# Performance work log

Hardware: AMD Instinct MI355X
Metric: run time of the kernel (lower is better)

## Reference

```python
import jax, jax.numpy as jnp
import numpy as np

B, N, M, C = 256, 2048, 64, 512
OUT = 3 * M + 6  # fc_write output: [M,1,1,3,1,M,M]


def setup_inputs() -> dict:
    key = jax.random.key(0)
    k0, k1, k2, k3, k4 = jax.random.split(key, 5)
    xavier = 1.4 * np.sqrt(6.0 / (C + OUT))  # xavier_uniform gain=1.4 scale
    return {
        "h": jax.random.normal(k0, (B, C), jnp.float32),
        "w_prev": jax.nn.softmax(jax.random.normal(k1, (B, N), jnp.float32), axis=1),
        "memory": jax.random.normal(k2, (B, N, M), jnp.float32),
        "W": jax.random.uniform(k3, (OUT, C), jnp.float32, -xavier, xavier),
        "b": 0.01 * jax.random.normal(k4, (OUT,), jnp.float32),
    }


def reference(h, w_prev, memory, W, b):
    # controller projection + split
    o = h @ W.T + b  # [B, 3M+6]
    bounds = np.cumsum([M, 1, 1, 3, 1, M])
    k, beta, g, s, gamma, e, a = jnp.split(o, bounds, axis=1)
    beta = jax.nn.softplus(beta)            # [B,1]
    g = jax.nn.sigmoid(g)                   # [B,1]
    s = jax.nn.softmax(s, axis=1)           # [B,3] shift weights {-1,0,+1}
    gamma = 1.0 + jax.nn.softplus(gamma)    # [B,1]
    e = jax.nn.sigmoid(e)                   # [B,M]

    # content addressing: cosine similarity + softmax
    mem_e = memory + 1e-16
    k_e = k + 1e-16
    sim = jnp.einsum('bnm,bm->bn', mem_e, k_e)
    denom = jnp.maximum(
        jnp.linalg.norm(mem_e, axis=-1) * jnp.linalg.norm(k_e, axis=-1, keepdims=True),
        1e-8,
    )
    w_c = jax.nn.softmax(beta * sim / denom, axis=1)  # [B,N]

    # interpolation gate
    w_g = g * w_c + (1.0 - g) * w_prev

    # circular shift convolution (3 taps)
    w_t = (jnp.roll(w_g, 1, axis=1) * s[:, 0:1]
           + w_g * s[:, 1:2]
           + jnp.roll(w_g, -1, axis=1) * s[:, 2:3])

    # sharpening
    w_s = w_t ** gamma
    w = w_s / (jnp.sum(w_s, axis=1, keepdims=True) + 1e-16)  # [B,N]

    # erase/add memory write
    erase = jnp.einsum('bn,bm->bnm', w, e)
    add = jnp.einsum('bn,bm->bnm', w, a)
    mem_new = memory * (1.0 - erase) + add
    return w, mem_new
```

## Files before the change

kernel.cpp:

```cpp
#include <hip/hip_runtime.h>
#include <stdint.h>

#define BB   256
#define NN   2048
#define MM   64
#define CC   512
#define OUTD 198

#define CHUNK_F 4096
#define NCH     32

typedef float vf4 __attribute__((ext_vector_type(4)));

__device__ __forceinline__ float softplusf(float x) {
    return x > 20.f ? x : log1pf(expf(x));
}
__device__ __forceinline__ float sigmoidf(float x) {
    return 1.f / (1.f + expf(-x));
}

__device__ __forceinline__ void dma16(const float* g, float* l) {
    __builtin_amdgcn_global_load_lds(
        (const __attribute__((address_space(1))) uint32_t*)g,
        (__attribute__((address_space(3))) uint32_t*)l, 16, 0, 0);
}

__device__ __forceinline__ void bar_lds() {
    asm volatile("s_waitcnt lgkmcnt(0)" ::: "memory");
    __builtin_amdgcn_sched_barrier(0);
    __builtin_amdgcn_s_barrier();
    __builtin_amdgcn_sched_barrier(0);
}

__global__ __launch_bounds__(1024, 4) void k_fused(
        const float* __restrict__ h, const float* __restrict__ Wm,
        const float* __restrict__ bias, const float* __restrict__ w_prev,
        const float* __restrict__ mem, float* __restrict__ w_out,
        float* __restrict__ mem_out) {
    __shared__ __align__(16) float stage[2][CHUNK_F];
    __shared__ float hs[CC];
    __shared__ float os[OUTD];
    __shared__ __align__(16) float kk[MM];
    __shared__ __align__(16) float ee[MM];
    __shared__ __align__(16) float aa[MM];
    __shared__ float sc[8];
    __shared__ float lgs[NN];
    __shared__ float wg[NN];
    __shared__ float wprev_s[NN];
    __shared__ float red[16];

    const int b  = blockIdx.x;
    const int t  = threadIdx.x;
    const int ln = t & 63;
    const int wv = t >> 6;
    const int seg  = ln & 15;
    const int rsub = ln >> 4;

    const float* mb = mem + (size_t)b * (NN * MM);

    float hv = 0.f;
    if (t < CC) hv = h[(size_t)b * CC + t];
    const float wp0 = w_prev[(size_t)b * NN + t];
    const float wp1 = w_prev[(size_t)b * NN + t + 1024];
    dma16(mb + 0 * CHUNK_F + wv * 256 + ln * 4, &stage[0][wv * 256]);
    dma16(mb + 1 * CHUNK_F + wv * 256 + ln * 4, &stage[1][wv * 256]);
    if (t < CC) hs[t] = hv;
    wprev_s[t] = wp0;
    wprev_s[t + 1024] = wp1;
    bar_lds();

    if (t < 4 * OUTD) {
        const int row = t >> 2, l4 = t & 3;
        const float* wr = Wm + (size_t)row * CC + 4 * l4;
        float acc = 0.f;
        #pragma unroll
        for (int c = 0; c < CC; c += 16) {
            const float4 p = *(const float4*)(wr + c);
            const int hb = c + 4 * l4;
            acc += p.x * hs[hb] + p.y * hs[hb + 1] + p.z * hs[hb + 2] + p.w * hs[hb + 3];
        }
        acc += __shfl_xor(acc, 1, 64);
        acc += __shfl_xor(acc, 2, 64);
        if (l4 == 0) os[row] = acc + bias[row];
    }
    bar_lds();

    if (t < 64) {
        const float kv = os[t] + 1e-16f;
        kk[t] = kv;
        float ss = kv * kv;
        #pragma unroll
        for (int off = 32; off; off >>= 1) ss += __shfl_xor(ss, off, 64);
        if (t == 0) sc[3] = sqrtf(ss);
    } else if (t < 128) {
        const int m = t - 64;
        ee[m] = sigmoidf(os[70 + m]);
        aa[m] = os[134 + m];
    } else if (t == 128) {
        sc[0] = softplusf(os[64]);
    } else if (t == 129) {
        sc[1] = sigmoidf(os[65]);
    } else if (t == 130) {
        sc[2] = 1.f + softplusf(os[69]);
    } else if (t == 131) {
        const float x0 = os[66], x1 = os[67], x2 = os[68];
        const float mx = fmaxf(x0, fmaxf(x1, x2));
        const float e0 = expf(x0 - mx), e1 = expf(x1 - mx), e2 = expf(x2 - mx);
        const float inv = 1.f / (e0 + e1 + e2);
        sc[4] = e0 * inv; sc[5] = e1 * inv; sc[6] = e2 * inv;
    }
    bar_lds();

    {
        const float kv0 = kk[4 * seg + 0], kv1 = kk[4 * seg + 1];
        const float kv2 = kk[4 * seg + 2], kv3 = kk[4 * seg + 3];
        const float beta = sc[0], knorm = sc[3];
        for (int c = 0; c < NCH; ++c) {
            if (c < NCH - 1) { asm volatile("s_waitcnt vmcnt(1)" ::: "memory"); }
            else             { asm volatile("s_waitcnt vmcnt(0)" ::: "memory"); }
            __builtin_amdgcn_sched_barrier(0);
            const float4 p = *(const float4*)&stage[c & 1][wv * 256 + ln * 4];
            const float m0 = p.x + 1e-16f, m1 = p.y + 1e-16f;
            const float m2 = p.z + 1e-16f, m3 = p.w + 1e-16f;
            float dot = m0 * kv0 + m1 * kv1 + m2 * kv2 + m3 * kv3;
            float ss  = m0 * m0 + m1 * m1 + m2 * m2 + m3 * m3;
            #pragma unroll
            for (int off = 1; off < 16; off <<= 1) {
                dot += __shfl_xor(dot, off, 64);
                ss  += __shfl_xor(ss,  off, 64);
            }
            if (seg == 0)
                lgs[c * 64 + wv * 4 + rsub] =
                    beta * dot / fmaxf(sqrtf(ss) * knorm, 1e-8f);
            if (c + 2 < NCH)
                dma16(mb + (size_t)(c + 2) * CHUNK_F + wv * 256 + ln * 4,
                      &stage[c & 1][wv * 256]);
        }
    }
    dma16(mb + 0 * CHUNK_F + wv * 256 + ln * 4, &stage[0][wv * 256]);
    dma16(mb + 1 * CHUNK_F + wv * 256 + ln * 4, &stage[1][wv * 256]);
    bar_lds();

    const float g = sc[1], gamma = sc[2];
    const float s0 = sc[4], s1 = sc[5], s2 = sc[6];

    float v0 = lgs[t], v1 = lgs[t + 1024];
    float lmax = fmaxf(v0, v1);
    #pragma unroll
    for (int off = 32; off; off >>= 1) lmax = fmaxf(lmax, __shfl_xor(lmax, off, 64));
    if (ln == 0) red[wv] = lmax;
    bar_lds();
    float mx = red[0];
    #pragma unroll
    for (int i = 1; i < 16; ++i) mx = fmaxf(mx, red[i]);
    bar_lds();

    v0 = expf(v0 - mx); v1 = expf(v1 - mx);
    float lsum = v0 + v1;
    #pragma unroll
    for (int off = 32; off; off >>= 1) lsum += __shfl_xor(lsum, off, 64);
    if (ln == 0) red[wv] = lsum;
    bar_lds();
    float tot = 0.f;
    #pragma unroll
    for (int i = 0; i < 16; ++i) tot += red[i];
    bar_lds();
    const float inv = 1.f / tot;

    wg[t]        = g * (v0 * inv) + (1.f - g) * wprev_s[t];
    wg[t + 1024] = g * (v1 * inv) + (1.f - g) * wprev_s[t + 1024];
    bar_lds();

    float ws0, ws1;
    {
        const int n0 = t;
        const float wt0 = wg[(n0 + NN - 1) & (NN - 1)] * s0 + wg[n0] * s1
                        + wg[(n0 + 1) & (NN - 1)] * s2;
        ws0 = (wt0 > 0.f) ? exp2f(gamma * log2f(wt0)) : 0.f;
        const int n1 = t + 1024;
        const float wt1 = wg[(n1 - 1) & (NN - 1)] * s0 + wg[n1] * s1
                        + wg[(n1 + 1) & (NN - 1)] * s2;
        ws1 = (wt1 > 0.f) ? exp2f(gamma * log2f(wt1)) : 0.f;
    }
    float psum = ws0 + ws1;
    #pragma unroll
    for (int off = 32; off; off >>= 1) psum += __shfl_xor(psum, off, 64);
    if (ln == 0) red[wv] = psum;
    bar_lds();
    float ptot = 0.f;
    #pragma unroll
    for (int i = 0; i < 16; ++i) ptot += red[i];
    const float invp = 1.f / (ptot + 1e-16f);

    const float wf0 = ws0 * invp, wf1 = ws1 * invp;
    lgs[t] = wf0;
    lgs[t + 1024] = wf1;
    w_out[(size_t)b * NN + t] = wf0;
    w_out[(size_t)b * NN + t + 1024] = wf1;
    bar_lds();

    {
        const vf4 ev = *(const vf4*)&ee[4 * seg];
        const vf4 av = *(const vf4*)&aa[4 * seg];
        float* ob = mem_out + (size_t)b * (NN * MM);
        for (int c = 0; c < NCH; ++c) {
            if (c < NCH - 1) { asm volatile("s_waitcnt vmcnt(2)" ::: "memory"); }
            else             { asm volatile("s_waitcnt vmcnt(0)" ::: "memory"); }
            __builtin_amdgcn_sched_barrier(0);
            const float wq = lgs[c * 64 + wv * 4 + rsub];
            const float4 p = *(const float4*)&stage[c & 1][wv * 256 + ln * 4];
            vf4 o;
            o.x = p.x * (1.f - wq * ev.x) + wq * av.x;
            o.y = p.y * (1.f - wq * ev.y) + wq * av.y;
            o.z = p.z * (1.f - wq * ev.z) + wq * av.z;
            o.w = p.w * (1.f - wq * ev.w) + wq * av.w;
            __builtin_nontemporal_store(
                o, (vf4*)(ob + (size_t)c * CHUNK_F + wv * 256 + ln * 4));
            if (c + 2 < NCH)
                dma16(mb + (size_t)(c + 2) * CHUNK_F + wv * 256 + ln * 4,
                      &stage[c & 1][wv * 256]);
        }
    }
}

extern "C" void kernel_launch(void* const* d_in, const int* in_sizes, int n_in,
                              void* d_out, int out_size, void* d_ws, size_t ws_size,
                              hipStream_t stream) {
    const float* h      = (const float*)d_in[0];
    const float* w_prev = (const float*)d_in[1];
    const float* memory = (const float*)d_in[2];
    const float* W      = (const float*)d_in[3];
    const float* bias   = (const float*)d_in[4];
    float* out = (float*)d_out;

    float* w_out   = out;
    float* mem_out = out + (size_t)BB * NN;

    k_fused<<<BB, 1024, 0, stream>>>(h, W, bias, w_prev, memory, w_out, mem_out);
}
```

Measured before the change: 269.0 us.

## Deepen memory DMA pipeline to four stages and fuse softmax max into similarity pass

Grows the LDS staging ring from two to four chunk buffers, so up to four global-to-LDS loads stay in flight during both the similarity pass and the erase/add pass. Chunks 0-3 for the second pass are prefetched at the end of the first loop by wrapping the index. The softmax max is now tracked inside the similarity loop, which removes a separate reduction pass and several barriers; a second reduction buffer drops another barrier. The larger LDS footprint (64KB of staging) may lower the number of resident blocks per CU, and the hand-tuned vmcnt counts must match the number of outstanding stores and loads exactly.

```diff
diff --git a/kernel.cpp b/kernel.cpp
--- a/kernel.cpp
+++ b/kernel.cpp
@@ -25,6 +25,11 @@
         (__attribute__((address_space(3))) uint32_t*)l, 16, 0, 0);
 }
 
+#define WAITV(N) do { \
+    asm volatile("s_waitcnt vmcnt(" #N ")" ::: "memory"); \
+    __builtin_amdgcn_sched_barrier(0); \
+} while (0)
+
 __device__ __forceinline__ void bar_lds() {
     asm volatile("s_waitcnt lgkmcnt(0)" ::: "memory");
     __builtin_amdgcn_sched_barrier(0);
@@ -37,7 +42,7 @@
         const float* __restrict__ bias, const float* __restrict__ w_prev,
         const float* __restrict__ mem, float* __restrict__ w_out,
         float* __restrict__ mem_out) {
-    __shared__ __align__(16) float stage[2][CHUNK_F];
+    __shared__ __align__(16) float stage[4][CHUNK_F];
     __shared__ float hs[CC];
     __shared__ float os[OUTD];
     __shared__ __align__(16) float kk[MM];
@@ -48,6 +53,7 @@
     __shared__ float wg[NN];
     __shared__ float wprev_s[NN];
     __shared__ float red[16];
+    __shared__ float red2[16];
 
     const int b  = blockIdx.x;
     const int t  = threadIdx.x;
@@ -83,6 +89,8 @@
         acc += __shfl_xor(acc, 2, 64);
         if (l4 == 0) os[row] = acc + bias[row];
     }
+    dma16(mb + 2 * CHUNK_F + wv * 256 + ln * 4, &stage[2][wv * 256]);
+    dma16(mb + 3 * CHUNK_F + wv * 256 + ln * 4, &stage[3][wv * 256]);
     bar_lds();
 
     if (t < 64) {
@@ -111,15 +119,14 @@
     }
     bar_lds();
 
+    float wmax = -1e30f;
     {
         const float kv0 = kk[4 * seg + 0], kv1 = kk[4 * seg + 1];
         const float kv2 = kk[4 * seg + 2], kv3 = kk[4 * seg + 3];
         const float beta = sc[0], knorm = sc[3];
         for (int c = 0; c < NCH; ++c) {
-            if (c < NCH - 1) { asm volatile("s_waitcnt vmcnt(1)" ::: "memory"); }
-            else             { asm volatile("s_waitcnt vmcnt(0)" ::: "memory"); }
-            __builtin_amdgcn_sched_barrier(0);
-            const float4 p = *(const float4*)&stage[c & 1][wv * 256 + ln * 4];
+            WAITV(3);
+            const float4 p = *(const float4*)&stage[c & 3][wv * 256 + ln * 4];
             const float m0 = p.x + 1e-16f, m1 = p.y + 1e-16f;
             const float m2 = p.z + 1e-16f, m3 = p.w + 1e-16f;
             float dot = m0 * kv0 + m1 * kv1 + m2 * kv2 + m3 * kv3;
@@ -129,42 +136,33 @@
                 dot += __shfl_xor(dot, off, 64);
                 ss  += __shfl_xor(ss,  off, 64);
             }
-            if (seg == 0)
-                lgs[c * 64 + wv * 4 + rsub] =
-                    beta * dot / fmaxf(sqrtf(ss) * knorm, 1e-8f);
-            if (c + 2 < NCH)
-                dma16(mb + (size_t)(c + 2) * CHUNK_F + wv * 256 + ln * 4,
-                      &stage[c & 1][wv * 256]);
+            const float lgv = beta * dot / fmaxf(sqrtf(ss) * knorm, 1e-8f);
+            wmax = fmaxf(wmax, lgv);
+            if (seg == 0) lgs[c * 64 + wv * 4 + rsub] = lgv;
+            dma16(mb + (size_t)((c + 4) & 31) * CHUNK_F + wv * 256 + ln * 4,
+                  &stage[(c + 4) & 3][wv * 256]);
         }
     }
-    dma16(mb + 0 * CHUNK_F + wv * 256 + ln * 4, &stage[0][wv * 256]);
-    dma16(mb + 1 * CHUNK_F + wv * 256 + ln * 4, &stage[1][wv * 256]);
+    wmax = fmaxf(wmax, __shfl_xor(wmax, 16, 64));
+    wmax = fmaxf(wmax, __shfl_xor(wmax, 32, 64));
+    if (ln == 0) red[wv] = wmax;
     bar_lds();
 
     const float g = sc[1], gamma = sc[2];
     const float s0 = sc[4], s1 = sc[5], s2 = sc[6];
 
-    float v0 = lgs[t], v1 = lgs[t + 1024];
-    float lmax = fmaxf(v0, v1);
-    #pragma unroll
-    for (int off = 32; off; off >>= 1) lmax = fmaxf(lmax, __shfl_xor(lmax, off, 64));
-    if (ln == 0) red[wv] = lmax;
-    bar_lds();
     float mx = red[0];
     #pragma unroll
     for (int i = 1; i < 16; ++i) mx = fmaxf(mx, red[i]);
-    bar_lds();
-
-    v0 = expf(v0 - mx); v1 = expf(v1 - mx);
+    float v0 = expf(lgs[t] - mx), v1 = expf(lgs[t + 1024] - mx);
     float lsum = v0 + v1;
     #pragma unroll
     for (int off = 32; off; off >>= 1) lsum += __shfl_xor(lsum, off, 64);
-    if (ln == 0) red[wv] = lsum;
+    if (ln == 0) red2[wv] = lsum;
     bar_lds();
     float tot = 0.f;
     #pragma unroll
-    for (int i = 0; i < 16; ++i) tot += red[i];
-    bar_lds();
+    for (int i = 0; i < 16; ++i) tot += red2[i];
     const float inv = 1.f / tot;
 
     wg[t]        = g * (v0 * inv) + (1.f - g) * wprev_s[t];
@@ -203,12 +201,18 @@
         const vf4 ev = *(const vf4*)&ee[4 * seg];
         const vf4 av = *(const vf4*)&aa[4 * seg];
         float* ob = mem_out + (size_t)b * (NN * MM);
+        #pragma unroll
         for (int c = 0; c < NCH; ++c) {
-            if (c < NCH - 1) { asm volatile("s_waitcnt vmcnt(2)" ::: "memory"); }
-            else             { asm volatile("s_waitcnt vmcnt(0)" ::: "memory"); }
-            __builtin_amdgcn_sched_barrier(0);
+            if      (c == 0) WAITV(5);
+            else if (c == 1) WAITV(6);
+            else if (c == 2) WAITV(7);
+            else if (c == 3) WAITV(8);
+            else if (c == 29) WAITV(5);
+            else if (c == 30) WAITV(4);
+            else if (c == 31) WAITV(3);
+            else             WAITV(6);
             const float wq = lgs[c * 64 + wv * 4 + rsub];
-            const float4 p = *(const float4*)&stage[c & 1][wv * 256 + ln * 4];
+            const float4 p = *(const float4*)&stage[c & 3][wv * 256 + ln * 4];
             vf4 o;
             o.x = p.x * (1.f - wq * ev.x) + wq * av.x;
             o.y = p.y * (1.f - wq * ev.y) + wq * av.y;
@@ -216,9 +220,9 @@
             o.w = p.w * (1.f - wq * ev.w) + wq * av.w;
             __builtin_nontemporal_store(
                 o, (vf4*)(ob + (size_t)c * CHUNK_F + wv * 256 + ln * 4));
-            if (c + 2 < NCH)
-                dma16(mb + (size_t)(c + 2) * CHUNK_F + wv * 256 + ln * 4,
-                      &stage[c & 1][wv * 256]);
+            if (c < NCH - 4)
+                dma16(mb + (size_t)(c + 4) * CHUNK_F + wv * 256 + ln * 4,
+                      &stage[(c + 4) & 3][wv * 256]);
         }
     }
 }
```

After: 272.9 us. No clear change (+1.4%).
